# Optimization experiments

Measured on AMD Instinct MI355X. Metric: run time of the kernel, lower is better.

Reference implementation:

```python
import jax, jax.numpy as jnp
import numpy as np

B, N, HD = 4, 2048, 256
E, T = 4096, 1024
PROPAG_STEPS = 5
ALPHA_MAX = 0.2
LN_EPS = 1e-5


def setup_inputs() -> dict:
    key = jax.random.key(0)
    ks = jax.random.split(key, 16)
    s_in, s_h = (2.0 * HD) ** -0.5, HD ** -0.5
    return {
        "attr_matrix": jax.random.normal(ks[0], (B, N, 1), dtype=jnp.float32),
        "adj_matrix": jax.random.uniform(ks[1], (B, N, N), dtype=jnp.float32),
        # ggnn.linear_i: 1 -> HD
        "W_i": jax.random.normal(ks[2], (HD, 1), dtype=jnp.float32),
        "b_i": jnp.zeros((HD,), dtype=jnp.float32),
        # ggnn.gru: GRUCell(input=2*HD, hidden=HD), torch gate order r,z,n
        "W_ih": jax.random.normal(ks[3], (3 * HD, 2 * HD), dtype=jnp.float32) * s_in,
        "b_ih": jnp.zeros((3 * HD,), dtype=jnp.float32),
        "W_hh": jax.random.normal(ks[4], (3 * HD, HD), dtype=jnp.float32) * s_h,
        "b_hh": jnp.zeros((3 * HD,), dtype=jnp.float32),
        # ggnn.linear_o: HD -> 1
        "W_o": jax.random.normal(ks[5], (1, HD), dtype=jnp.float32) * s_h,
        "b_o": jnp.zeros((1,), dtype=jnp.float32),
        # topo buffers (incidence-like, kept small to mimic sparse +/-1 matrices)
        "B1": jax.random.normal(ks[6], (N, E), dtype=jnp.float32) * 0.02,
        "B2": jax.random.normal(ks[7], (E, T), dtype=jnp.float32) * 0.02,
        # topo trainables
        "proj_W": jax.random.normal(ks[8], (HD, HD), dtype=jnp.float32) * s_h,
        "ln_gamma": jnp.ones((HD,), dtype=jnp.float32),
        "ln_beta": jnp.zeros((HD,), dtype=jnp.float32),
        "alpha_raw": jnp.float32(-2.0),
    }


def _gru_cell(x, h, W_ih, b_ih, W_hh, b_hh):
    # x: [B,N,2H], h: [B,N,H]; torch GRUCell gate order: r, z, n
    gx = jnp.einsum('bni,gi->bng', x, W_ih) + b_ih
    gh = jnp.einsum('bnh,gh->bng', h, W_hh) + b_hh
    xr, xz, xn = jnp.split(gx, 3, axis=-1)
    hr, hz, hn = jnp.split(gh, 3, axis=-1)
    r = jax.nn.sigmoid(xr + hr)
    z = jax.nn.sigmoid(xz + hz)
    n = jnp.tanh(xn + r * hn)
    return (1.0 - z) * n + z * h


def _layernorm(x, gamma, beta):
    mu = jnp.mean(x, axis=-1, keepdims=True)
    var = jnp.mean(jnp.square(x - mu), axis=-1, keepdims=True)
    return (x - mu) * jax.lax.rsqrt(var + LN_EPS) * gamma + beta


def reference(attr_matrix, adj_matrix, W_i, b_i, W_ih, b_ih, W_hh, b_hh,
              W_o, b_o, B1, B2, proj_W, ln_gamma, ln_beta, alpha_raw):
    A_in = adj_matrix                      # [B,N,N]
    A_out = jnp.swapaxes(adj_matrix, -2, -1)
    # linear_i + relu
    h = jax.nn.relu(jnp.einsum('bnc,hc->bnh', attr_matrix, W_i) + b_i)  # [B,N,H]
    # GGNN propagation
    for _ in range(PROPAG_STEPS):
        a_in = jnp.einsum('bnm,bmh->bnh', A_in, h)
        a_out = jnp.einsum('bnm,bmh->bnh', A_out, h)
        h = _gru_cell(jnp.concatenate((a_in, a_out), axis=-1), h,
                      W_ih, b_ih, W_hh, b_hh)
    # topo residual: dH = B1 (L1 (B1^T h)), L1 = B1^T B1 + B2 B2^T
    L1 = B1.T @ B1 + B2 @ B2.T             # [E,E]
    E_feat = jnp.einsum('ne,bnh->beh', B1, h)       # B1^T H
    E_topo = jnp.einsum('ef,bfh->beh', L1, E_feat)
    dH = jnp.einsum('ne,beh->bnh', B1, E_topo)
    dH = _layernorm(jax.nn.relu(jnp.einsum('bnh,oh->bno', dH, proj_W)),
                    ln_gamma, ln_beta)
    alpha = ALPHA_MAX * jax.nn.sigmoid(alpha_raw)
    h = h + alpha * dH
    # linear_o -> [B,N] (squeeze(0) is a no-op for B>1)
    anomaly = (jnp.einsum('bnh,oh->bno', h, W_o) + b_o)[..., 0]
    return anomaly
```

## Files before the change

kernel.cpp:

```cpp
#include <hip/hip_runtime.h>


typedef __bf16 bf16x8 __attribute__((ext_vector_type(8)));
typedef float f32x4 __attribute__((ext_vector_type(4)));

#define BM 128
#define BN 128
#define BK 16

__device__ __forceinline__ unsigned short bf16rne(float x)
{
    unsigned u = __float_as_uint(x);
    return (unsigned short)((u + 0x7FFFu + ((u >> 16) & 1u)) >> 16);
}
__device__ __forceinline__ float bf2f(unsigned short h)
{
    return __uint_as_float((unsigned)h << 16);
}

__device__ __forceinline__ void split2(float x, unsigned short& hi, unsigned short& lo)
{
    hi = bf16rne(x);
    lo = bf16rne(x - bf2f(hi));
}

__device__ __forceinline__ void split3(float x, unsigned short& hi,
                                       unsigned short& md, unsigned short& lo)
{
    hi = bf16rne(x);
    float r = x - bf2f(hi);
    md = bf16rne(r);
    lo = bf16rne(r - bf2f(md));
}

__device__ __forceinline__ void gload_lds16(const unsigned short* g, unsigned short* l)
{
    __builtin_amdgcn_global_load_lds(
        (const __attribute__((address_space(1))) void*)g,
        (__attribute__((address_space(3))) void*)l, 16, 0, 0);
}

__device__ __forceinline__ void stage2(const unsigned short* g, unsigned short* l, int K)
{
    gload_lds16(g, l);
    gload_lds16(g + (size_t)32 * K, l + 2048);
}

template<int SPLIT>
__device__ __forceinline__ void mm_loop64(
    const unsigned short* ag0, const unsigned short* ag1, const unsigned short* ag2,
    const unsigned short* bg0, const unsigned short* bg1, const unsigned short* bg2,
    int K, unsigned short* LDS, int tid, f32x4 (&acc)[2][2])
{
    constexpr int NT = (SPLIT == 0) ? 1 : ((SPLIT == 4) ? 3 : 2);
    constexpr int TSZ = 4096;

    int lane = tid & 63, r16 = lane & 15, g = lane >> 4, s7 = r16 & 7;
    int wv = tid >> 6, wr = wv >> 1, wc = wv & 1;
    int arow = (wr * 32 + r16) * 128;
    int brow = (wc * 32 + r16) * 128;
    unsigned short* lA = LDS + (tid >> 6) * 512;
    unsigned short* lB = LDS + NT * TSZ + (tid >> 6) * 512;
    const char* Ab = (const char*)LDS;
    const char* Bb = (const char*)(LDS + NT * TSZ);

    for (int k0 = 0; k0 < K; k0 += 64) {
        stage2(ag0 + k0, lA, K);
        if constexpr (NT > 1) stage2(ag1 + k0, lA + TSZ, K);
        if constexpr (NT > 2) stage2(ag2 + k0, lA + 2 * TSZ, K);
        stage2(bg0 + k0, lB, K);
        if constexpr (NT > 1) stage2(bg1 + k0, lB + TSZ, K);
        if constexpr (NT > 2) stage2(bg2 + k0, lB + 2 * TSZ, K);
        __syncthreads();
#pragma unroll
        for (int ks = 0; ks < 2; ++ks) {
            int tt = ((ks * 4 + g) ^ s7) * 16;
            bf16x8 a0[2], a1[2], a2[2], b0[2], b1[2], b2[2];
#pragma unroll
            for (int mi = 0; mi < 2; ++mi) {
                a0[mi] = *(const bf16x8*)(Ab + arow + mi * 2048 + tt);
                if constexpr (NT > 1)
                    a1[mi] = *(const bf16x8*)(Ab + TSZ * 2 + arow + mi * 2048 + tt);
                if constexpr (NT > 2)
                    a2[mi] = *(const bf16x8*)(Ab + TSZ * 4 + arow + mi * 2048 + tt);
            }
#pragma unroll
            for (int ni = 0; ni < 2; ++ni) {
                b0[ni] = *(const bf16x8*)(Bb + brow + ni * 2048 + tt);
                if constexpr (NT > 1)
                    b1[ni] = *(const bf16x8*)(Bb + TSZ * 2 + brow + ni * 2048 + tt);
                if constexpr (NT > 2)
                    b2[ni] = *(const bf16x8*)(Bb + TSZ * 4 + brow + ni * 2048 + tt);
            }
#pragma unroll
            for (int mi = 0; mi < 2; ++mi)
#pragma unroll
                for (int ni = 0; ni < 2; ++ni) {
                    if constexpr (SPLIT == 4) {
                        acc[mi][ni] = __builtin_amdgcn_mfma_f32_16x16x32_bf16(
                            a2[mi], b0[ni], acc[mi][ni], 0, 0, 0);
                        acc[mi][ni] = __builtin_amdgcn_mfma_f32_16x16x32_bf16(
                            a0[mi], b2[ni], acc[mi][ni], 0, 0, 0);
                        acc[mi][ni] = __builtin_amdgcn_mfma_f32_16x16x32_bf16(
                            a1[mi], b1[ni], acc[mi][ni], 0, 0, 0);
                        acc[mi][ni] = __builtin_amdgcn_mfma_f32_16x16x32_bf16(
                            a1[mi], b0[ni], acc[mi][ni], 0, 0, 0);
                        acc[mi][ni] = __builtin_amdgcn_mfma_f32_16x16x32_bf16(
                            a0[mi], b1[ni], acc[mi][ni], 0, 0, 0);
                    } else if constexpr (SPLIT == 1 || SPLIT == 2) {
                        acc[mi][ni] = __builtin_amdgcn_mfma_f32_16x16x32_bf16(
                            a1[mi], b0[ni], acc[mi][ni], 0, 0, 0);
                        acc[mi][ni] = __builtin_amdgcn_mfma_f32_16x16x32_bf16(
                            a0[mi], b1[ni], acc[mi][ni], 0, 0, 0);
                        if constexpr (SPLIT == 2)
                            acc[mi][ni] = __builtin_amdgcn_mfma_f32_16x16x32_bf16(
                                a1[mi], b1[ni], acc[mi][ni], 0, 0, 0);
                    }
                    acc[mi][ni] = __builtin_amdgcn_mfma_f32_16x16x32_bf16(
                        a0[mi], b0[ni], acc[mi][ni], 0, 0, 0);
                }
        }
        __syncthreads();
    }
}

template<int SPLIT, int OBF>
__global__ __launch_bounds__(256, 2) void mm_bf16(
    const unsigned short* __restrict__ Ah, const unsigned short* __restrict__ A2,
    const unsigned short* __restrict__ A3,
    const unsigned short* __restrict__ Bh, const unsigned short* __restrict__ B2,
    const unsigned short* __restrict__ B3,
    int K, const float* __restrict__ bias, const float* __restrict__ Cacc,
    void* __restrict__ Cout, int ldc)
{
    constexpr int NT = (SPLIT == 0) ? 1 : ((SPLIT == 4) ? 3 : 2);
    __shared__ unsigned short LDS[2 * NT * 4096];
    int tid = threadIdx.x;

    unsigned nwg = gridDim.x * gridDim.y;
    unsigned lin = blockIdx.y * gridDim.x + blockIdx.x;
    unsigned wk = ((nwg & 7) == 0) ? (lin & 7) * (nwg >> 3) + (lin >> 3) : lin;
    unsigned bx = wk % gridDim.x, by = wk / gridDim.x;

    int m0 = by * 64, n0 = bx * 64;
    int rp = tid >> 3, sl8 = ((tid & 7) ^ (rp & 7)) * 8;
    const unsigned short* ag0 = Ah + (size_t)(m0 + rp) * K + sl8;
    const unsigned short* ag1 = (NT > 1) ? A2 + (size_t)(m0 + rp) * K + sl8 : nullptr;
    const unsigned short* ag2 = (NT > 2) ? A3 + (size_t)(m0 + rp) * K + sl8 : nullptr;
    const unsigned short* bg0 = Bh + (size_t)(n0 + rp) * K + sl8;
    const unsigned short* bg1 = (NT > 1) ? B2 + (size_t)(n0 + rp) * K + sl8 : nullptr;
    const unsigned short* bg2 = (NT > 2) ? B3 + (size_t)(n0 + rp) * K + sl8 : nullptr;

    f32x4 acc[2][2];
#pragma unroll
    for (int mi = 0; mi < 2; ++mi)
#pragma unroll
        for (int ni = 0; ni < 2; ++ni)
            acc[mi][ni] = (f32x4){0.f, 0.f, 0.f, 0.f};

    mm_loop64<SPLIT>(ag0, ag1, ag2, bg0, bg1, bg2, K, LDS, tid, acc);

    int lane = tid & 63, r16 = lane & 15, g = lane >> 4;
    int wv = tid >> 6, wr = wv >> 1, wc = wv & 1;
#pragma unroll
    for (int mi = 0; mi < 2; ++mi) {
#pragma unroll
        for (int ni = 0; ni < 2; ++ni) {
            int col = n0 + wc * 32 + ni * 16 + r16;
            float badd = bias ? bias[col] : 0.f;
#pragma unroll
            for (int j = 0; j < 4; ++j) {
                int row = m0 + wr * 32 + mi * 16 + g * 4 + j;
                float v = acc[mi][ni][j] + badd;
                if (Cacc) v += Cacc[(size_t)row * ldc + col];
                if (OBF)
                    ((unsigned short*)Cout)[(size_t)row * ldc + col] = bf16rne(v);
                else
                    ((float*)Cout)[(size_t)row * ldc + col] = v;
            }
        }
    }
}

__global__ __launch_bounds__(256, 2) void mm_step1(
    const unsigned short* __restrict__ AhHi, const unsigned short* __restrict__ AhLo,
    const unsigned short* __restrict__ AtHi, const unsigned short* __restrict__ AtLo,
    const unsigned short* __restrict__ hTh, const unsigned short* __restrict__ hTl,
    unsigned short* __restrict__ Xhi, unsigned short* __restrict__ Xmd,
    unsigned short* __restrict__ Xlo,
    const unsigned short* __restrict__ hrmh, const unsigned short* __restrict__ hrml,
    const unsigned short* __restrict__ WhhH, const unsigned short* __restrict__ WhhL,
    const float* __restrict__ b_hh, float* __restrict__ ghb)
{
    __shared__ unsigned short LDS[16384];
    int tid = threadIdx.x;
    unsigned bid = blockIdx.x;
    int lane = tid & 63, r16 = lane & 15, g = lane >> 4;
    int wv = tid >> 6, wr = wv >> 1, wc = wv & 1;
    int rp = tid >> 3, sl8 = ((tid & 7) ^ (rp & 7)) * 8;

    if (bid < 1024) {
        unsigned lin = bid;
        unsigned wk = (lin & 7) * 128 + (lin >> 3);
        unsigned bz = wk >> 7, rem = wk & 127, by = rem >> 2, bx = rem & 3;
        int b = bz >> 1, wio = bz & 1;
        const unsigned short* Ahp = (wio ? AtHi : AhHi) + (size_t)b * 4194304;
        const unsigned short* Alp = (wio ? AtLo : AhLo) + (size_t)b * 4194304;
        size_t boff = (size_t)(b * 256 + bx * 64) * 2048;
        int m0 = by * 64;
        const int K = 2048;
        const unsigned short* ag0 = Ahp + (size_t)(m0 + rp) * K + sl8;
        const unsigned short* ag1 = Alp + (size_t)(m0 + rp) * K + sl8;
        const unsigned short* bg0 = hTh + boff + (size_t)rp * K + sl8;
        const unsigned short* bg1 = hTl + boff + (size_t)rp * K + sl8;

        f32x4 acc[2][2];
#pragma unroll
        for (int mi = 0; mi < 2; ++mi)
#pragma unroll
            for (int ni = 0; ni < 2; ++ni)
                acc[mi][ni] = (f32x4){0.f, 0.f, 0.f, 0.f};

        mm_loop64<1>(ag0, ag1, nullptr, bg0, bg1, nullptr, K, LDS, tid, acc);

        float* T = reinterpret_cast<float*>(LDS);
#pragma unroll
        for (int mi = 0; mi < 2; ++mi)
#pragma unroll
            for (int ni = 0; ni < 2; ++ni)
#pragma unroll
                for (int j = 0; j < 4; ++j)
                    T[(wr * 32 + mi * 16 + g * 4 + j) * 68 +
                      wc * 32 + ni * 16 + r16] = acc[mi][ni][j];
        __syncthreads();

        int row = tid >> 2, fq = tid & 3;
        const float* src = T + row * 68 + fq * 16;
        unsigned hw[8], mw[8], lw[8];
#pragma unroll
        for (int e = 0; e < 8; ++e) {
            unsigned short h0, m0_, l0, h1, m1_, l1;
            split3(src[2 * e], h0, m0_, l0);
            split3(src[2 * e + 1], h1, m1_, l1);
            hw[e] = (unsigned)h0 | ((unsigned)h1 << 16);
            mw[e] = (unsigned)m0_ | ((unsigned)m1_ << 16);
            lw[e] = (unsigned)l0 | ((unsigned)l1 << 16);
        }
        size_t base = ((size_t)(m0 + row) * 4 + b) * 512 + wio * 256 + bx * 64 + fq * 16;
        ((uint4*)(Xhi + base))[0] = (uint4){hw[0], hw[1], hw[2], hw[3]};
        ((uint4*)(Xhi + base))[1] = (uint4){hw[4], hw[5], hw[6], hw[7]};
        ((uint4*)(Xmd + base))[0] = (uint4){mw[0], mw[1], mw[2], mw[3]};
        ((uint4*)(Xmd + base))[1] = (uint4){mw[4], mw[5], mw[6], mw[7]};
        ((uint4*)(Xlo + base))[0] = (uint4){lw[0], lw[1], lw[2], lw[3]};
        ((uint4*)(Xlo + base))[1] = (uint4){lw[4], lw[5], lw[6], lw[7]};
    } else {
        unsigned gidx = bid - 1024;
        unsigned by = gidx / 12, bx = gidx % 12;
        int m0 = by * 64, n0 = bx * 64;
        const int K = 256;
        const unsigned short* ag0 = hrmh + (size_t)(m0 + rp) * K + sl8;
        const unsigned short* ag1 = hrml + (size_t)(m0 + rp) * K + sl8;
        const unsigned short* bg0 = WhhH + (size_t)(n0 + rp) * K + sl8;
        const unsigned short* bg1 = WhhL + (size_t)(n0 + rp) * K + sl8;

        f32x4 acc[2][2];
#pragma unroll
        for (int mi = 0; mi < 2; ++mi)
#pragma unroll
            for (int ni = 0; ni < 2; ++ni)
                acc[mi][ni] = (f32x4){0.f, 0.f, 0.f, 0.f};

        mm_loop64<2>(ag0, ag1, nullptr, bg0, bg1, nullptr, K, LDS, tid, acc);

#pragma unroll
        for (int mi = 0; mi < 2; ++mi) {
#pragma unroll
            for (int ni = 0; ni < 2; ++ni) {
                int col = n0 + wc * 32 + ni * 16 + r16;
                float badd = b_hh[col];
#pragma unroll
                for (int j = 0; j < 4; ++j) {
                    int row = m0 + wr * 32 + mi * 16 + g * 4 + j;
                    ghb[(size_t)row * 768 + col] = acc[mi][ni][j] + badd;
                }
            }
        }
    }
}

__global__ __launch_bounds__(256, 2) void gemm_f32(
    const float* __restrict__ A, const float* __restrict__ B, float* __restrict__ C,
    int M, int N, int K, int lda, int ldb, int ldc,
    long sA, long sB, long sC,
    const float* __restrict__ bias, int ta, int tb, int accum)
{
    int bz = blockIdx.z;
    int taEff = ta;
    if (ta == 2) {
        int b = bz >> 1, w = bz & 1;
        A += (long)b * sA; B += (long)b * sB; C += (long)b * sC + w * 256;
        taEff = w;
    } else {
        A += (long)bz * sA; B += (long)bz * sB; C += (long)bz * sC;
    }
    int m0 = blockIdx.y * BM, n0 = blockIdx.x * BN;

    __shared__ float As[BK][BM + 4];
    __shared__ float Bs[BK][BN + 4];

// ... 94 lines not shown
        ushort4 h, l;
        split2(v.x, h.x, l.x); split2(v.y, h.y, l.y);
        split2(v.z, h.z, l.z); split2(v.w, h.w, l.w);
        size_t o = (size_t)z * 4194304 + (size_t)(i0 + r) * 2048 + j0 + tx * 4;
        *(ushort4*)(nhi + o) = h; *(ushort4*)(nlo + o) = l;
        t[r][tx * 4 + 0] = v.x; t[r][tx * 4 + 1] = v.y;
        t[r][tx * 4 + 2] = v.z; t[r][tx * 4 + 3] = v.w;
    }
    __syncthreads();
#pragma unroll
    for (int i = 0; i < 4; ++i) {
        int r = ty * 4 + i;
        ushort4 h, l;
        split2(t[tx * 4 + 0][r], h.x, l.x);
        split2(t[tx * 4 + 1][r], h.y, l.y);
        split2(t[tx * 4 + 2][r], h.z, l.z);
        split2(t[tx * 4 + 3][r], h.w, l.w);
        size_t o = (size_t)z * 4194304 + (size_t)(j0 + r) * 2048 + i0 + tx * 4;
        *(ushort4*)(thi + o) = h; *(ushort4*)(tlo + o) = l;
    }
}

__global__ void split_h(const float* __restrict__ h,
                        unsigned short* __restrict__ hi, unsigned short* __restrict__ lo,
                        unsigned short* __restrict__ hrmh, unsigned short* __restrict__ hrml)
{
    __shared__ float t[64][68];
    int f0 = blockIdx.x * 64, n0 = blockIdx.y * 64;
    int tx = threadIdx.x & 15, ty = threadIdx.x >> 4;
#pragma unroll
    for (int i = 0; i < 4; ++i) {
        int r = ty * 4 + i;
        float4 v = *(const float4*)(h + (size_t)(n0 + r) * 1024 + f0 + tx * 4);
        t[r][tx * 4 + 0] = v.x; t[r][tx * 4 + 1] = v.y;
        t[r][tx * 4 + 2] = v.z; t[r][tx * 4 + 3] = v.w;
        if (hrmh) {
            ushort4 hh, ll;
            split2(v.x, hh.x, ll.x); split2(v.y, hh.y, ll.y);
            split2(v.z, hh.z, ll.z); split2(v.w, hh.w, ll.w);
            size_t o = (size_t)(n0 + r) * 1024 + f0 + tx * 4;
            *(ushort4*)(hrmh + o) = hh;
            *(ushort4*)(hrml + o) = ll;
        }
    }
    __syncthreads();
#pragma unroll
    for (int i = 0; i < 4; ++i) {
        int r = ty * 4 + i;
        ushort4 hh, ll;
        split2(t[tx * 4 + 0][r], hh.x, ll.x);
        split2(t[tx * 4 + 1][r], hh.y, ll.y);
        split2(t[tx * 4 + 2][r], hh.z, ll.z);
        split2(t[tx * 4 + 3][r], hh.w, ll.w);
        size_t o = (size_t)(f0 + r) * 2048 + n0 + tx * 4;
        *(ushort4*)(hi + o) = hh; *(ushort4*)(lo + o) = ll;
    }
}

__global__ void split_t(const float* __restrict__ in, unsigned short* __restrict__ outN,
                        unsigned short* __restrict__ outT, int R, int C)
{
    __shared__ float t[64][68];
    int i0 = blockIdx.y * 64, j0 = blockIdx.x * 64;
    int tx = threadIdx.x & 15, ty = threadIdx.x >> 4;
#pragma unroll
    for (int i = 0; i < 4; ++i) {
        int r = ty * 4 + i;
        float4 v = *(const float4*)(in + (size_t)(i0 + r) * C + j0 + tx * 4);
        ushort4 hh;
        hh.x = bf16rne(v.x); hh.y = bf16rne(v.y);
        hh.z = bf16rne(v.z); hh.w = bf16rne(v.w);
        *(ushort4*)(outN + (size_t)(i0 + r) * C + j0 + tx * 4) = hh;
        t[r][tx * 4 + 0] = v.x; t[r][tx * 4 + 1] = v.y;
        t[r][tx * 4 + 2] = v.z; t[r][tx * 4 + 3] = v.w;
    }
    __syncthreads();
#pragma unroll
    for (int i = 0; i < 4; ++i) {
        int r = ty * 4 + i;
        ushort4 hh;
        hh.x = bf16rne(t[tx * 4 + 0][r]);
        hh.y = bf16rne(t[tx * 4 + 1][r]);
        hh.z = bf16rne(t[tx * 4 + 2][r]);
        hh.w = bf16rne(t[tx * 4 + 3][r]);
        *(ushort4*)(outT + (size_t)(j0 + r) * R + i0 + tx * 4) = hh;
    }
}

__global__ void split_w3(const float* __restrict__ Wih, const float* __restrict__ Whh,
                         const float* __restrict__ pj,
                         unsigned short* __restrict__ WihH, unsigned short* __restrict__ WihM,
                         unsigned short* __restrict__ WihL,
                         unsigned short* __restrict__ WhhH, unsigned short* __restrict__ WhhL,
                         unsigned short* __restrict__ pjH)
{
    int i = blockIdx.x * 256 + threadIdx.x;
    if (i < 393216) {
        unsigned short h, m, l;
        split3(Wih[i], h, m, l);
        WihH[i] = h; WihM[i] = m; WihL[i] = l;
    } else if (i < 589824) {
        int j = i - 393216;
        unsigned short h, l;
        split2(Whh[j], h, l);
        WhhH[j] = h; WhhL[j] = l;
    } else {
        int j = i - 589824;
        pjH[j] = bf16rne(pj[j]);
    }
}

__global__ __launch_bounds__(256, 3) void adj_mfma(
    const unsigned short* __restrict__ AhHi, const unsigned short* __restrict__ AhLo,
    const unsigned short* __restrict__ AtHi, const unsigned short* __restrict__ AtLo,
    const unsigned short* __restrict__ hTHi, const unsigned short* __restrict__ hTLo,
    float* __restrict__ c0, float* __restrict__ c1, float* __restrict__ c2)
{
    __shared__ unsigned short As[8192];
    __shared__ unsigned short Bs[8192];
    int tid = threadIdx.x;
    int bz = blockIdx.z;
    int region = bz >> 3, bw = bz & 7, b = bw >> 1, w = bw & 1;
    const unsigned short* Abase =
        (region == 2) ? (w ? AtLo : AhLo) : (w ? AtHi : AhHi);
    Abase += (size_t)b * 4194304;
    const unsigned short* Bbase = (region == 1) ? hTLo : hTHi;
    float* Cb = (region == 0) ? c0 : (region == 1 ? c1 : c2);

    int m0 = blockIdx.y * 128;
    int f0 = b * 256 + blockIdx.x * 128;

// ... 183 lines not shown
    const float* B1    = (const float*)d_in[10];
    const float* B2    = (const float*)d_in[11];
    const float* projW = (const float*)d_in[12];
    const float* gamma = (const float*)d_in[13];
    const float* beta  = (const float*)d_in[14];
    const float* araw  = (const float*)d_in[15];
    float* out = (float*)d_out;

    char* wsb = (char*)d_ws;
    dim3 blk(256);

    const size_t REQ1 = 0xD400000;
    const size_t REQ2 = 0xD000000;

    if (ws_size >= REQ1) {
        float* hbuf = (float*)(wsb);
        float* gxb  = (float*)(wsb + 0x0800000);
        unsigned short* hrmh = (unsigned short*)(wsb + 0x0800000);
        unsigned short* hrml = (unsigned short*)(wsb + 0x0C00000);
        unsigned short* hTh  = (unsigned short*)(wsb + 0x1800000);
        unsigned short* hTl  = (unsigned short*)(wsb + 0x1C00000);
        float* ghb  = (float*)(wsb + 0x2000000);
        unsigned short* Xhi = (unsigned short*)(wsb + 0x3800000);
        unsigned short* Xmd = (unsigned short*)(wsb + 0x4000000);
        unsigned short* Xlo = (unsigned short*)(wsb + 0x4800000);
        unsigned short* Wih_h = (unsigned short*)(wsb + 0x5000000);
        unsigned short* Wih_m = (unsigned short*)(wsb + 0x50C0000);
        unsigned short* Wih_l = (unsigned short*)(wsb + 0x5180000);
        unsigned short* Whh_h = (unsigned short*)(wsb + 0x5240000);
        unsigned short* Whh_l = (unsigned short*)(wsb + 0x52A0000);
        unsigned short* pjh   = (unsigned short*)(wsb + 0x5300000);
        char* R1 = wsb + 0x5400000;
        unsigned short* AhHi = (unsigned short*)(R1);
        unsigned short* AhLo = (unsigned short*)(R1 + 0x2000000);
        unsigned short* AtHi = (unsigned short*)(R1 + 0x4000000);
        unsigned short* AtLo = (unsigned short*)(R1 + 0x6000000);
        unsigned short* B1h = (unsigned short*)(R1);
        unsigned short* B1T = (unsigned short*)(R1 + 0x1000000);
        unsigned short* B2h = (unsigned short*)(R1 + 0x2000000);
        unsigned short* B2T = (unsigned short*)(R1 + 0x2800000);
        unsigned short* uTb = (unsigned short*)(R1 + 0x3000000);
        unsigned short* pTb = (unsigned short*)(R1 + 0x3800000);
        unsigned short* rTb = (unsigned short*)(R1 + 0x3C00000);
        unsigned short* qTb = (unsigned short*)(R1 + 0x3E00000);
        float* qTf = gxb;
        unsigned short* dHb = (unsigned short*)(wsb + 0x1800000);
        float* dPb = ghb;

        init_h<<<dim3(2048, 4), blk, 0, stream>>>(attr, W_i, b_i, hbuf);
        split_adj<<<dim3(32, 32, 4), blk, 0, stream>>>(adj, AhHi, AhLo, AtHi, AtLo);
        split_w3<<<dim3(2560), blk, 0, stream>>>(W_ih, W_hh, projW,
            Wih_h, Wih_m, Wih_l, Whh_h, Whh_l, pjh);

        for (int step = 0; step < 5; ++step) {
            split_h<<<dim3(16, 32), blk, 0, stream>>>(hbuf, hTh, hTl, hrmh, hrml);
            mm_step1<<<dim3(2560), blk, 0, stream>>>(
                AhHi, AhLo, AtHi, AtLo, hTh, hTl, Xhi, Xmd, Xlo,
                hrmh, hrml, Whh_h, Whh_l, b_hh, ghb);
            mm_bf16<4, 0><<<dim3(12, 128), blk, 0, stream>>>(
                Xhi, Xmd, Xlo, Wih_h, Wih_m, Wih_l,
                512, b_ih, nullptr, gxb, 768);
            gru_ew<<<dim3(2048, 4), blk, 0, stream>>>(gxb, ghb, hbuf);
        }

        split_h<<<dim3(16, 32), blk, 0, stream>>>(hbuf, hTh, hTl, nullptr, nullptr);
        split_t<<<dim3(64, 32), blk, 0, stream>>>(B1, B1h, B1T, 2048, 4096);
        split_t<<<dim3(16, 64), blk, 0, stream>>>(B2, B2h, B2T, 4096, 1024);
        mm_bf16<0, 1><<<dim3(64, 16), blk, 0, stream>>>(
            hTh, nullptr, nullptr, B1T, nullptr, nullptr,
            2048, nullptr, nullptr, uTb, 4096);
        mm_bf16<0, 1><<<dim3(32, 16), blk, 0, stream>>>(
            uTb, nullptr, nullptr, B1h, nullptr, nullptr,
            4096, nullptr, nullptr, pTb, 2048);
        mm_bf16<0, 1><<<dim3(16, 16), blk, 0, stream>>>(
            uTb, nullptr, nullptr, B2T, nullptr, nullptr,
            4096, nullptr, nullptr, rTb, 1024);
        mm_bf16<0, 0><<<dim3(64, 16), blk, 0, stream>>>(
            pTb, nullptr, nullptr, B1T, nullptr, nullptr,
            2048, nullptr, nullptr, qTf, 4096);
        mm_bf16<0, 1><<<dim3(64, 16), blk, 0, stream>>>(
            rTb, nullptr, nullptr, B2h, nullptr, nullptr,
            1024, nullptr, qTf, qTb, 4096);
        mm_bf16<0, 1><<<dim3(16, 32), blk, 0, stream>>>(
            B1h, nullptr, nullptr, qTb, nullptr, nullptr,
            4096, nullptr, nullptr, dHb, 1024);
        mm_bf16<0, 0><<<dim3(4, 128), blk, 0, stream>>>(
            dHb, nullptr, nullptr, pjh, nullptr, nullptr,
            256, nullptr, nullptr, dPb, 256);

        ln_out<<<dim3(2048, 4), blk, 0, stream>>>(dPb, gamma, beta, araw,
                                                  hbuf, W_o, b_o, out);
        return;
    }

    float* hbuf = (float*)(wsb);
    float* xbuf = (float*)(wsb + 0x800000);
    float* gxb  = (float*)(wsb + 0x1800000);
    float* ghb  = (float*)(wsb + 0x3000000);
    unsigned short* AhHi = (unsigned short*)(wsb + 0x4800000);
    unsigned short* AhLo = (unsigned short*)(wsb + 0x6800000);
    unsigned short* AtHi = (unsigned short*)(wsb + 0x8800000);
    unsigned short* AtLo = (unsigned short*)(wsb + 0xA800000);
    unsigned short* hTHi = (unsigned short*)(wsb + 0xC800000);
    unsigned short* hTLo = (unsigned short*)(wsb + 0xCC00000);

    float* ub  = xbuf;
    float* pb  = gxb;
    float* qb  = gxb + (1 << 21);
    float* rb  = ghb;
    float* dHr = ghb + (1 << 20);
    float* dPb = ghb + 3 * (1 << 20);

    bool mfma_path = (ws_size >= REQ2);

    init_h<<<dim3(2048, 4), blk, 0, stream>>>(attr, W_i, b_i, hbuf);

    if (mfma_path)
        split_adj<<<dim3(32, 32, 4), blk, 0, stream>>>(adj, AhHi, AhLo, AtHi, AtLo);

    for (int step = 0; step < 5; ++step) {
        if (mfma_path) {
            split_h<<<dim3(16, 32), blk, 0, stream>>>(hbuf, hTHi, hTLo, nullptr, nullptr);
            adj_mfma<<<dim3(2, 16, 24), blk, 0, stream>>>(
                AhHi, AhLo, AtHi, AtLo, hTHi, hTLo, xbuf, gxb, ghb);
            reduce3<<<dim3(4096), blk, 0, stream>>>(
                (float4*)xbuf, (const float4*)gxb, (const float4*)ghb);
        } else {
            gemm_f32<<<dim3(2, 16, 8), blk, 0, stream>>>(
                adj, hbuf, xbuf, 2048, 256, 2048, 2048, 1024, 2048,
                (long)2048 * 2048, 256, 512, nullptr, 2, 0, 0);
        }
        gemm_f32<<<dim3(6, 64, 1), blk, 0, stream>>>(
            xbuf, W_ih, gxb, 8192, 768, 512, 512, 512, 768,
            0, 0, 0, b_ih, 0, 1, 0);
        gemm_f32<<<dim3(6, 64, 1), blk, 0, stream>>>(
            hbuf, W_hh, ghb, 8192, 768, 256, 256, 256, 768,
            0, 0, 0, b_hh, 0, 1, 0);
        gru_ew<<<dim3(2048, 4), blk, 0, stream>>>(gxb, ghb, hbuf);
    }

    gemm_f32<<<dim3(8, 32, 1), blk, 0, stream>>>(
        B1, hbuf, ub, 4096, 1024, 2048, 4096, 1024, 1024, 0, 0, 0, nullptr, 1, 0, 0);
    gemm_f32<<<dim3(8, 16, 1), blk, 0, stream>>>(
        B1, ub, pb, 2048, 1024, 4096, 4096, 1024, 1024, 0, 0, 0, nullptr, 0, 0, 0);
    gemm_f32<<<dim3(8, 32, 1), blk, 0, stream>>>(
// ... 14 lines not shown
```

Before: 921.5 us.

## Switch split-precision MFMA GEMMs from bf16 to scaled fp16 hi/lo pairs

Replaces the bf16 two- and three-term operand splits with fp16 hi/lo pairs, where the lo part is scaled by 1024 and accumulated separately. This cuts the three-way W_ih/X split to two terms (three MFMAs instead of five) and drops the lo*lo term in the W_hh GEMM. It also removes the middle split buffers and their stores. fp16's extra mantissa bits are meant to keep accuracy, at the risk of fp16 range overflow or underflow on inputs with large or tiny magnitudes.

```diff
diff --git a/kernel.cpp b/kernel.cpp
--- a/kernel.cpp
+++ b/kernel.cpp
@@ -1,12 +1,15 @@
 #include <hip/hip_runtime.h>
+#include <hip/hip_fp16.h>
 
 
 typedef __bf16 bf16x8 __attribute__((ext_vector_type(8)));
+typedef _Float16 f16x8 __attribute__((ext_vector_type(8)));
 typedef float f32x4 __attribute__((ext_vector_type(4)));
 
 #define BM 128
 #define BN 128
 #define BK 16
+#define LO_INV (1.f / 1024.f)
 
 __device__ __forceinline__ unsigned short bf16rne(float x)
 {
@@ -17,20 +20,24 @@
 {
     return __uint_as_float((unsigned)h << 16);
 }
-
 __device__ __forceinline__ void split2(float x, unsigned short& hi, unsigned short& lo)
 {
     hi = bf16rne(x);
     lo = bf16rne(x - bf2f(hi));
 }
 
-__device__ __forceinline__ void split3(float x, unsigned short& hi,
-                                       unsigned short& md, unsigned short& lo)
-{
-    hi = bf16rne(x);
-    float r = x - bf2f(hi);
-    md = bf16rne(r);
-    lo = bf16rne(r - bf2f(md));
+__device__ __forceinline__ unsigned short f16r(float x)
+{
+    return __half_as_ushort(__float2half(x));
+}
+__device__ __forceinline__ float f16f(unsigned short u)
+{
+    return __half2float(__ushort_as_half(u));
+}
+__device__ __forceinline__ void splitf(float x, unsigned short& hi, unsigned short& lo)
+{
+    hi = f16r(x);
+    lo = f16r((x - f16f(hi)) * 1024.f);
 }
 
 __device__ __forceinline__ void gload_lds16(const unsigned short* g, unsigned short* l)
@@ -47,12 +54,13 @@
 }
 
 template<int SPLIT>
-__device__ __forceinline__ void mm_loop64(
-    const unsigned short* ag0, const unsigned short* ag1, const unsigned short* ag2,
-    const unsigned short* bg0, const unsigned short* bg1, const unsigned short* bg2,
-    int K, unsigned short* LDS, int tid, f32x4 (&acc)[2][2])
-{
-    constexpr int NT = (SPLIT == 0) ? 1 : ((SPLIT == 4) ? 3 : 2);
+__device__ __forceinline__ void mm_loop64f(
+    const unsigned short* ag0, const unsigned short* ag1,
+    const unsigned short* bg0, const unsigned short* bg1,
+    int K, unsigned short* LDS, int tid,
+    f32x4 (&acc0)[2][2], f32x4 (&acc1)[2][2])
+{
+    constexpr int NT = SPLIT ? 2 : 1;
     constexpr int TSZ = 4096;
 
     int lane = tid & 63, r16 = lane & 15, g = lane >> 4, s7 = r16 & 7;
@@ -66,74 +74,52 @@
 
     for (int k0 = 0; k0 < K; k0 += 64) {
         stage2(ag0 + k0, lA, K);
-        if constexpr (NT > 1) stage2(ag1 + k0, lA + TSZ, K);
-        if constexpr (NT > 2) stage2(ag2 + k0, lA + 2 * TSZ, K);
+        if constexpr (SPLIT) stage2(ag1 + k0, lA + TSZ, K);
         stage2(bg0 + k0, lB, K);
-        if constexpr (NT > 1) stage2(bg1 + k0, lB + TSZ, K);
-        if constexpr (NT > 2) stage2(bg2 + k0, lB + 2 * TSZ, K);
+        if constexpr (SPLIT) stage2(bg1 + k0, lB + TSZ, K);
         __syncthreads();
 #pragma unroll
         for (int ks = 0; ks < 2; ++ks) {
             int tt = ((ks * 4 + g) ^ s7) * 16;
-            bf16x8 a0[2], a1[2], a2[2], b0[2], b1[2], b2[2];
+            f16x8 a0[2], a1[2], b0[2], b1[2];
 #pragma unroll
             for (int mi = 0; mi < 2; ++mi) {
-                a0[mi] = *(const bf16x8*)(Ab + arow + mi * 2048 + tt);
-                if constexpr (NT > 1)
-                    a1[mi] = *(const bf16x8*)(Ab + TSZ * 2 + arow + mi * 2048 + tt);
-                if constexpr (NT > 2)
-                    a2[mi] = *(const bf16x8*)(Ab + TSZ * 4 + arow + mi * 2048 + tt);
+                a0[mi] = *(const f16x8*)(Ab + arow + mi * 2048 + tt);
+                if constexpr (SPLIT)
+                    a1[mi] = *(const f16x8*)(Ab + TSZ * 2 + arow + mi * 2048 + tt);
             }
 #pragma unroll
             for (int ni = 0; ni < 2; ++ni) {
-                b0[ni] = *(const bf16x8*)(Bb + brow + ni * 2048 + tt);
-                if constexpr (NT > 1)
-                    b1[ni] = *(const bf16x8*)(Bb + TSZ * 2 + brow + ni * 2048 + tt);
-                if constexpr (NT > 2)
-                    b2[ni] = *(const bf16x8*)(Bb + TSZ * 4 + brow + ni * 2048 + tt);
+                b0[ni] = *(const f16x8*)(Bb + brow + ni * 2048 + tt);
+                if constexpr (SPLIT)
+                    b1[ni] = *(const f16x8*)(Bb + TSZ * 2 + brow + ni * 2048 + tt);
             }
 #pragma unroll
             for (int mi = 0; mi < 2; ++mi)
 #pragma unroll
                 for (int ni = 0; ni < 2; ++ni) {
-                    if constexpr (SPLIT == 4) {
-                        acc[mi][ni] = __builtin_amdgcn_mfma_f32_16x16x32_bf16(
-                            a2[mi], b0[ni], acc[mi][ni], 0, 0, 0);
-                        acc[mi][ni] = __builtin_amdgcn_mfma_f32_16x16x32_bf16(
-                            a0[mi], b2[ni], acc[mi][ni], 0, 0, 0);
-                        acc[mi][ni] = __builtin_amdgcn_mfma_f32_16x16x32_bf16(
-                            a1[mi], b1[ni], acc[mi][ni], 0, 0, 0);
-                        acc[mi][ni] = __builtin_amdgcn_mfma_f32_16x16x32_bf16(
-                            a1[mi], b0[ni], acc[mi][ni], 0, 0, 0);
-                        acc[mi][ni] = __builtin_amdgcn_mfma_f32_16x16x32_bf16(
-                            a0[mi], b1[ni], acc[mi][ni], 0, 0, 0);
-                    } else if constexpr (SPLIT == 1 || SPLIT == 2) {
-                        acc[mi][ni] = __builtin_amdgcn_mfma_f32_16x16x32_bf16(
-                            a1[mi], b0[ni], acc[mi][ni], 0, 0, 0);
-                        acc[mi][ni] = __builtin_amdgcn_mfma_f32_16x16x32_bf16(
-                            a0[mi], b1[ni], acc[mi][ni], 0, 0, 0);
-                        if constexpr (SPLIT == 2)
-                            acc[mi][ni] = __builtin_amdgcn_mfma_f32_16x16x32_bf16(
-                                a1[mi], b1[ni], acc[mi][ni], 0, 0, 0);
+                    if constexpr (SPLIT) {
+                        acc1[mi][ni] = __builtin_amdgcn_mfma_f32_16x16x32_f16(
+                            a1[mi], b0[ni], acc1[mi][ni], 0, 0, 0);
+                        acc1[mi][ni] = __builtin_amdgcn_mfma_f32_16x16x32_f16(
+                            a0[mi], b1[ni], acc1[mi][ni], 0, 0, 0);
                     }
-                    acc[mi][ni] = __builtin_amdgcn_mfma_f32_16x16x32_bf16(
-                        a0[mi], b0[ni], acc[mi][ni], 0, 0, 0);
+                    acc0[mi][ni] = __builtin_amdgcn_mfma_f32_16x16x32_f16(
+                        a0[mi], b0[ni], acc0[mi][ni], 0, 0, 0);
                 }
         }
         __syncthreads();
     }
 }
 
-template<int SPLIT, int OBF>
-__global__ __launch_bounds__(256, 2) void mm_bf16(
-    const unsigned short* __restrict__ Ah, const unsigned short* __restrict__ A2,
-    const unsigned short* __restrict__ A3,
-    const unsigned short* __restrict__ Bh, const unsigned short* __restrict__ B2,
-    const unsigned short* __restrict__ B3,
+template<int SPLIT, int OF16>
+__global__ __launch_bounds__(256, 2) void mm_f16(
+    const unsigned short* __restrict__ Ah, const unsigned short* __restrict__ Al,
+    const unsigned short* __restrict__ Bh, const unsigned short* __restrict__ Bl,
     int K, const float* __restrict__ bias, const float* __restrict__ Cacc,
     void* __restrict__ Cout, int ldc)
 {
-    constexpr int NT = (SPLIT == 0) ? 1 : ((SPLIT == 4) ? 3 : 2);
+    constexpr int NT = SPLIT ? 2 : 1;
     __shared__ unsigned short LDS[2 * NT * 4096];
     int tid = threadIdx.x;
 
@@ -145,20 +131,20 @@
     int m0 = by * 64, n0 = bx * 64;
     int rp = tid >> 3, sl8 = ((tid & 7) ^ (rp & 7)) * 8;
     const unsigned short* ag0 = Ah + (size_t)(m0 + rp) * K + sl8;
-    const unsigned short* ag1 = (NT > 1) ? A2 + (size_t)(m0 + rp) * K + sl8 : nullptr;
-    const unsigned short* ag2 = (NT > 2) ? A3 + (size_t)(m0 + rp) * K + sl8 : nullptr;
+    const unsigned short* ag1 = SPLIT ? Al + (size_t)(m0 + rp) * K + sl8 : nullptr;
     const unsigned short* bg0 = Bh + (size_t)(n0 + rp) * K + sl8;
-    const unsigned short* bg1 = (NT > 1) ? B2 + (size_t)(n0 + rp) * K + sl8 : nullptr;
-    const unsigned short* bg2 = (NT > 2) ? B3 + (size_t)(n0 + rp) * K + sl8 : nullptr;
-
-    f32x4 acc[2][2];
+    const unsigned short* bg1 = SPLIT ? Bl + (size_t)(n0 + rp) * K + sl8 : nullptr;
+
+    f32x4 acc0[2][2], acc1[2][2];
 #pragma unroll
     for (int mi = 0; mi < 2; ++mi)
 #pragma unroll
-        for (int ni = 0; ni < 2; ++ni)
-            acc[mi][ni] = (f32x4){0.f, 0.f, 0.f, 0.f};
-
-    mm_loop64<SPLIT>(ag0, ag1, ag2, bg0, bg1, bg2, K, LDS, tid, acc);
+        for (int ni = 0; ni < 2; ++ni) {
+            acc0[mi][ni] = (f32x4){0.f, 0.f, 0.f, 0.f};
+            acc1[mi][ni] = (f32x4){0.f, 0.f, 0.f, 0.f};
+        }
+
+    mm_loop64f<SPLIT>(ag0, ag1, bg0, bg1, K, LDS, tid, acc0, acc1);
 
     int lane = tid & 63, r16 = lane & 15, g = lane >> 4;
     int wv = tid >> 6, wr = wv >> 1, wc = wv & 1;
@@ -171,10 +157,11 @@
 #pragma unroll
             for (int j = 0; j < 4; ++j) {
                 int row = m0 + wr * 32 + mi * 16 + g * 4 + j;
-                float v = acc[mi][ni][j] + badd;
+                float v = acc0[mi][ni][j] + badd;
+                if (SPLIT) v += acc1[mi][ni][j] * LO_INV;
                 if (Cacc) v += Cacc[(size_t)row * ldc + col];
-                if (OBF)
-                    ((unsigned short*)Cout)[(size_t)row * ldc + col] = bf16rne(v);
+                if (OF16)
+                    ((unsigned short*)Cout)[(size_t)row * ldc + col] = f16r(v);
                 else
                     ((float*)Cout)[(size_t)row * ldc + col] = v;
             }
@@ -182,12 +169,11 @@
     }
 }
 
-__global__ __launch_bounds__(256, 2) void mm_step1(
+__global__ __launch_bounds__(256, 2) void mm_step1f(
     const unsigned short* __restrict__ AhHi, const unsigned short* __restrict__ AhLo,
     const unsigned short* __restrict__ AtHi, const unsigned short* __restrict__ AtLo,
     const unsigned short* __restrict__ hTh, const unsigned short* __restrict__ hTl,
-    unsigned short* __restrict__ Xhi, unsigned short* __restrict__ Xmd,
-    unsigned short* __restrict__ Xlo,
+    unsigned short* __restrict__ Xhi, unsigned short* __restrict__ Xlo,
     const unsigned short* __restrict__ hrmh, const unsigned short* __restrict__ hrml,
     const unsigned short* __restrict__ WhhH, const unsigned short* __restrict__ WhhL,
     const float* __restrict__ b_hh, float* __restrict__ ghb)
@@ -199,9 +185,17 @@
     int wv = tid >> 6, wr = wv >> 1, wc = wv & 1;
     int rp = tid >> 3, sl8 = ((tid & 7) ^ (rp & 7)) * 8;
 
+    f32x4 acc0[2][2], acc1[2][2];
+#pragma unroll
+    for (int mi = 0; mi < 2; ++mi)
+#pragma unroll
+        for (int ni = 0; ni < 2; ++ni) {
+            acc0[mi][ni] = (f32x4){0.f, 0.f, 0.f, 0.f};
+            acc1[mi][ni] = (f32x4){0.f, 0.f, 0.f, 0.f};
+        }
+
     if (bid < 1024) {
-        unsigned lin = bid;
-        unsigned wk = (lin & 7) * 128 + (lin >> 3);
+        unsigned wk = (bid & 7) * 128 + (bid >> 3);
         unsigned bz = wk >> 7, rem = wk & 127, by = rem >> 2, bx = rem & 3;
         int b = bz >> 1, wio = bz & 1;
         const unsigned short* Ahp = (wio ? AtHi : AhHi) + (size_t)b * 4194304;
@@ -214,14 +208,7 @@
         const unsigned short* bg0 = hTh + boff + (size_t)rp * K + sl8;
         const unsigned short* bg1 = hTl + boff + (size_t)rp * K + sl8;
 
-        f32x4 acc[2][2];
-#pragma unroll
-        for (int mi = 0; mi < 2; ++mi)
-#pragma unroll
-            for (int ni = 0; ni < 2; ++ni)
-                acc[mi][ni] = (f32x4){0.f, 0.f, 0.f, 0.f};
-
-        mm_loop64<1>(ag0, ag1, nullptr, bg0, bg1, nullptr, K, LDS, tid, acc);
+        mm_loop64f<1>(ag0, ag1, bg0, bg1, K, LDS, tid, acc0, acc1);
 
         float* T = reinterpret_cast<float*>(LDS);
 #pragma unroll
@@ -231,26 +218,24 @@
 #pragma unroll
                 for (int j = 0; j < 4; ++j)
                     T[(wr * 32 + mi * 16 + g * 4 + j) * 68 +
-                      wc * 32 + ni * 16 + r16] = acc[mi][ni][j];
+                      wc * 32 + ni * 16 + r16] =
+                        acc0[mi][ni][j] + acc1[mi][ni][j] * LO_INV;
         __syncthreads();
 
         int row = tid >> 2, fq = tid & 3;
         const float* src = T + row * 68 + fq * 16;
-        unsigned hw[8], mw[8], lw[8];
+        unsigned hw[8], lw[8];
 #pragma unroll
         for (int e = 0; e < 8; ++e) {
-            unsigned short h0, m0_, l0, h1, m1_, l1;
-            split3(src[2 * e], h0, m0_, l0);
-            split3(src[2 * e + 1], h1, m1_, l1);
+            unsigned short h0, l0, h1, l1;
+            splitf(src[2 * e], h0, l0);
+            splitf(src[2 * e + 1], h1, l1);
             hw[e] = (unsigned)h0 | ((unsigned)h1 << 16);
-            mw[e] = (unsigned)m0_ | ((unsigned)m1_ << 16);
             lw[e] = (unsigned)l0 | ((unsigned)l1 << 16);
         }
         size_t base = ((size_t)(m0 + row) * 4 + b) * 512 + wio * 256 + bx * 64 + fq * 16;
         ((uint4*)(Xhi + base))[0] = (uint4){hw[0], hw[1], hw[2], hw[3]};
         ((uint4*)(Xhi + base))[1] = (uint4){hw[4], hw[5], hw[6], hw[7]};
-        ((uint4*)(Xmd + base))[0] = (uint4){mw[0], mw[1], mw[2], mw[3]};
-        ((uint4*)(Xmd + base))[1] = (uint4){mw[4], mw[5], mw[6], mw[7]};
         ((uint4*)(Xlo + base))[0] = (uint4){lw[0], lw[1], lw[2], lw[3]};
         ((uint4*)(Xlo + base))[1] = (uint4){lw[4], lw[5], lw[6], lw[7]};
     } else {
@@ -263,14 +248,7 @@
         const unsigned short* bg0 = WhhH + (size_t)(n0 + rp) * K + sl8;
         const unsigned short* bg1 = WhhL + (size_t)(n0 + rp) * K + sl8;
 
-        f32x4 acc[2][2];
-#pragma unroll
-        for (int mi = 0; mi < 2; ++mi)
-#pragma unroll
-            for (int ni = 0; ni < 2; ++ni)
-                acc[mi][ni] = (f32x4){0.f, 0.f, 0.f, 0.f};
-
-        mm_loop64<2>(ag0, ag1, nullptr, bg0, bg1, nullptr, K, LDS, tid, acc);
+        mm_loop64f<1>(ag0, ag1, bg0, bg1, K, LDS, tid, acc0, acc1);
 
 #pragma unroll
         for (int mi = 0; mi < 2; ++mi) {
@@ -281,10 +259,134 @@
 #pragma unroll
                 for (int j = 0; j < 4; ++j) {
                     int row = m0 + wr * 32 + mi * 16 + g * 4 + j;
-                    ghb[(size_t)row * 768 + col] = acc[mi][ni][j] + badd;
+                    ghb[(size_t)row * 768 + col] =
+                        acc0[mi][ni][j] + acc1[mi][ni][j] * LO_INV + badd;
                 }
             }
         }
+    }
+}
+
+__global__ void split_adj16(const float* __restrict__ adj,
+                            unsigned short* __restrict__ nhi, unsigned short* __restrict__ nlo,
+                            unsigned short* __restrict__ thi, unsigned short* __restrict__ tlo)
+{
+    __shared__ float t[64][68];
+    int z = blockIdx.z;
+    const float* src = adj + (size_t)z * 4194304;
+    int tx = threadIdx.x & 15, ty = threadIdx.x >> 4;
+    int i0 = blockIdx.y * 64, j0 = blockIdx.x * 64;
+#pragma unroll
+    for (int i = 0; i < 4; ++i) {
+        int r = ty * 4 + i;
+        float4 v = *(const float4*)(src + (size_t)(i0 + r) * 2048 + j0 + tx * 4);
+        ushort4 h, l;
+        splitf(v.x, h.x, l.x); splitf(v.y, h.y, l.y);
+        splitf(v.z, h.z, l.z); splitf(v.w, h.w, l.w);
+        size_t o = (size_t)z * 4194304 + (size_t)(i0 + r) * 2048 + j0 + tx * 4;
+        *(ushort4*)(nhi + o) = h; *(ushort4*)(nlo + o) = l;
+        t[r][tx * 4 + 0] = v.x; t[r][tx * 4 + 1] = v.y;
+        t[r][tx * 4 + 2] = v.z; t[r][tx * 4 + 3] = v.w;
+    }
+    __syncthreads();
+#pragma unroll
+    for (int i = 0; i < 4; ++i) {
+        int r = ty * 4 + i;
+        ushort4 h, l;
+        splitf(t[tx * 4 + 0][r], h.x, l.x);
+        splitf(t[tx * 4 + 1][r], h.y, l.y);
+        splitf(t[tx * 4 + 2][r], h.z, l.z);
+        splitf(t[tx * 4 + 3][r], h.w, l.w);
+        size_t o = (size_t)z * 4194304 + (size_t)(j0 + r) * 2048 + i0 + tx * 4;
+        *(ushort4*)(thi + o) = h; *(ushort4*)(tlo + o) = l;
+    }
+}
+
+__global__ void split_h16(const float* __restrict__ h,
+                          unsigned short* __restrict__ hi, unsigned short* __restrict__ lo,
+                          unsigned short* __restrict__ hrmh, unsigned short* __restrict__ hrml)
+{
+    __shared__ float t[64][68];
+    int f0 = blockIdx.x * 64, n0 = blockIdx.y * 64;
+    int tx = threadIdx.x & 15, ty = threadIdx.x >> 4;
+#pragma unroll
+    for (int i = 0; i < 4; ++i) {
+        int r = ty * 4 + i;
+        float4 v = *(const float4*)(h + (size_t)(n0 + r) * 1024 + f0 + tx * 4);
+        t[r][tx * 4 + 0] = v.x; t[r][tx * 4 + 1] = v.y;
+        t[r][tx * 4 + 2] = v.z; t[r][tx * 4 + 3] = v.w;
+        if (hrmh) {
+            ushort4 hh, ll;
+            splitf(v.x, hh.x, ll.x); splitf(v.y, hh.y, ll.y);
+            splitf(v.z, hh.z, ll.z); splitf(v.w, hh.w, ll.w);
+            size_t o = (size_t)(n0 + r) * 1024 + f0 + tx * 4;
+            *(ushort4*)(hrmh + o) = hh;
+            *(ushort4*)(hrml + o) = ll;
+        }
+    }
+    __syncthreads();
+#pragma unroll
+    for (int i = 0; i < 4; ++i) {
+        int r = ty * 4 + i;
+        ushort4 hh, ll;
+        splitf(t[tx * 4 + 0][r], hh.x, ll.x);
+        splitf(t[tx * 4 + 1][r], hh.y, ll.y);
+        splitf(t[tx * 4 + 2][r], hh.z, ll.z);
+        splitf(t[tx * 4 + 3][r], hh.w, ll.w);
+        size_t o = (size_t)(f0 + r) * 2048 + n0 + tx * 4;
+        *(ushort4*)(hi + o) = hh; *(ushort4*)(lo + o) = ll;
+    }
+}
+
+__global__ void split_t16(const float* __restrict__ in, unsigned short* __restrict__ outN,
+                          unsigned short* __restrict__ outT, int R, int C)
+{
+    __shared__ float t[64][68];
+    int i0 = blockIdx.y * 64, j0 = blockIdx.x * 64;
+    int tx = threadIdx.x & 15, ty = threadIdx.x >> 4;
+#pragma unroll
+    for (int i = 0; i < 4; ++i) {
+        int r = ty * 4 + i;
+        float4 v = *(const float4*)(in + (size_t)(i0 + r) * C + j0 + tx * 4);
+        ushort4 hh;
+        hh.x = f16r(v.x); hh.y = f16r(v.y);
+        hh.z = f16r(v.z); hh.w = f16r(v.w);
+        *(ushort4*)(outN + (size_t)(i0 + r) * C + j0 + tx * 4) = hh;
+        t[r][tx * 4 + 0] = v.x; t[r][tx * 4 + 1] = v.y;
+        t[r][tx * 4 + 2] = v.z; t[r][tx * 4 + 3] = v.w;
+    }
+    __syncthreads();
+#pragma unroll
+    for (int i = 0; i < 4; ++i) {
+        int r = ty * 4 + i;
+        ushort4 hh;
+        hh.x = f16r(t[tx * 4 + 0][r]);
+        hh.y = f16r(t[tx * 4 + 1][r]);
+        hh.z = f16r(t[tx * 4 + 2][r]);
+        hh.w = f16r(t[tx * 4 + 3][r]);
+        *(ushort4*)(outT + (size_t)(j0 + r) * R + i0 + tx * 4) = hh;
+    }
+}
+
+__global__ void split_w16(const float* __restrict__ Wih, const float* __restrict__ Whh,
+                          const float* __restrict__ pj,
+                          unsigned short* __restrict__ WihH, unsigned short* __restrict__ WihL,
+                          unsigned short* __restrict__ WhhH, unsigned short* __restrict__ WhhL,
+                          unsigned short* __restrict__ pjH)
+{
+    int i = blockIdx.x * 256 + threadIdx.x;
+    if (i < 393216) {
+        unsigned short h, l;
+        splitf(Wih[i], h, l);
+        WihH[i] = h; WihL[i] = l;
+    } else if (i < 589824) {
+        int j = i - 393216;
+        unsigned short h, l;
+        splitf(Whh[j], h, l);
+        WhhH[j] = h; WhhL[j] = l;
+    } else if (i < 655360) {
+        int j = i - 589824;
+        pjH[j] = f16r(pj[j]);
     }
 }
 
@@ -425,8 +527,7 @@
 }
 
 __global__ void split_h(const float* __restrict__ h,
-                        unsigned short* __restrict__ hi, unsigned short* __restrict__ lo,
-                        unsigned short* __restrict__ hrmh, unsigned short* __restrict__ hrml)
+                        unsigned short* __restrict__ hi, unsigned short* __restrict__ lo)
 {
     __shared__ float t[64][68];
     int f0 = blockIdx.x * 64, n0 = blockIdx.y * 64;
@@ -437,14 +538,6 @@
         float4 v = *(const float4*)(h + (size_t)(n0 + r) * 1024 + f0 + tx * 4);
         t[r][tx * 4 + 0] = v.x; t[r][tx * 4 + 1] = v.y;
         t[r][tx * 4 + 2] = v.z; t[r][tx * 4 + 3] = v.w;
-        if (hrmh) {
-            ushort4 hh, ll;
-            split2(v.x, hh.x, ll.x); split2(v.y, hh.y, ll.y);
-            split2(v.z, hh.z, ll.z); split2(v.w, hh.w, ll.w);
-            size_t o = (size_t)(n0 + r) * 1024 + f0 + tx * 4;
-            *(ushort4*)(hrmh + o) = hh;
-            *(ushort4*)(hrml + o) = ll;
-        }
     }
     __syncthreads();
 #pragma unroll
@@ -457,59 +550,6 @@
         split2(t[tx * 4 + 3][r], hh.w, ll.w);
         size_t o = (size_t)(f0 + r) * 2048 + n0 + tx * 4;
         *(ushort4*)(hi + o) = hh; *(ushort4*)(lo + o) = ll;
-    }
-}
-
-__global__ void split_t(const float* __restrict__ in, unsigned short* __restrict__ outN,
-                        unsigned short* __restrict__ outT, int R, int C)
-{
-    __shared__ float t[64][68];
-    int i0 = blockIdx.y * 64, j0 = blockIdx.x * 64;
-    int tx = threadIdx.x & 15, ty = threadIdx.x >> 4;
-#pragma unroll
-    for (int i = 0; i < 4; ++i) {
-        int r = ty * 4 + i;
-        float4 v = *(const float4*)(in + (size_t)(i0 + r) * C + j0 + tx * 4);
-        ushort4 hh;
-        hh.x = bf16rne(v.x); hh.y = bf16rne(v.y);
-        hh.z = bf16rne(v.z); hh.w = bf16rne(v.w);
-        *(ushort4*)(outN + (size_t)(i0 + r) * C + j0 + tx * 4) = hh;
-        t[r][tx * 4 + 0] = v.x; t[r][tx * 4 + 1] = v.y;
-        t[r][tx * 4 + 2] = v.z; t[r][tx * 4 + 3] = v.w;
-    }
-    __syncthreads();
-#pragma unroll
-    for (int i = 0; i < 4; ++i) {
-        int r = ty * 4 + i;
-        ushort4 hh;
-        hh.x = bf16rne(t[tx * 4 + 0][r]);
-        hh.y = bf16rne(t[tx * 4 + 1][r]);
-        hh.z = bf16rne(t[tx * 4 + 2][r]);
-        hh.w = bf16rne(t[tx * 4 + 3][r]);
-        *(ushort4*)(outT + (size_t)(j0 + r) * R + i0 + tx * 4) = hh;
-    }
-}
-
-__global__ void split_w3(const float* __restrict__ Wih, const float* __restrict__ Whh,
-                         const float* __restrict__ pj,
-                         unsigned short* __restrict__ WihH, unsigned short* __restrict__ WihM,
-                         unsigned short* __restrict__ WihL,
-                         unsigned short* __restrict__ WhhH, unsigned short* __restrict__ WhhL,
-                         unsigned short* __restrict__ pjH)
-{
-    int i = blockIdx.x * 256 + threadIdx.x;
-    if (i < 393216) {
-        unsigned short h, m, l;
-        split3(Wih[i], h, m, l);
-        WihH[i] = h; WihM[i] = m; WihL[i] = l;
-    } else if (i < 589824) {
-        int j = i - 393216;
-        unsigned short h, l;
-        split2(Whh[j], h, l);
-        WhhH[j] = h; WhhL[j] = l;
-    } else {
-        int j = i - 589824;
-        pjH[j] = bf16rne(pj[j]);
     }
 }
 
@@ -739,11 +779,9 @@
         unsigned short* hTl  = (unsigned short*)(wsb + 0x1C00000);
         float* ghb  = (float*)(wsb + 0x2000000);
         unsigned short* Xhi = (unsigned short*)(wsb + 0x3800000);
-        unsigned short* Xmd = (unsigned short*)(wsb + 0x4000000);
-        unsigned short* Xlo = (unsigned short*)(wsb + 0x4800000);
+        unsigned short* Xlo = (unsigned short*)(wsb + 0x4000000);
         unsigned short* Wih_h = (unsigned short*)(wsb + 0x5000000);
-        unsigned short* Wih_m = (unsigned short*)(wsb + 0x50C0000);
-        unsigned short* Wih_l = (unsigned short*)(wsb + 0x5180000);
+        unsigned short* Wih_l = (unsigned short*)(wsb + 0x50C0000);
         unsigned short* Whh_h = (unsigned short*)(wsb + 0x5240000);
         unsigned short* Whh_l = (unsigned short*)(wsb + 0x52A0000);
         unsigned short* pjh   = (unsigned short*)(wsb + 0x5300000);
@@ -765,45 +803,37 @@
         float* dPb = ghb;
 
         init_h<<<dim3(2048, 4), blk, 0, stream>>>(attr, W_i, b_i, hbuf);
-        split_adj<<<dim3(32, 32, 4), blk, 0, stream>>>(adj, AhHi, AhLo, AtHi, AtLo);
-        split_w3<<<dim3(2560), blk, 0, stream>>>(W_ih, W_hh, projW,
-            Wih_h, Wih_m, Wih_l, Whh_h, Whh_l, pjh);
+        split_adj16<<<dim3(32, 32, 4), blk, 0, stream>>>(adj, AhHi, AhLo, AtHi, AtLo);
+        split_w16<<<dim3(2560), blk, 0, stream>>>(W_ih, W_hh, projW,
+            Wih_h, Wih_l, Whh_h, Whh_l, pjh);
 
         for (int step = 0; step < 5; ++step) {
-            split_h<<<dim3(16, 32), blk, 0, stream>>>(hbuf, hTh, hTl, hrmh, hrml);
-            mm_step1<<<dim3(2560), blk, 0, stream>>>(
-                AhHi, AhLo, AtHi, AtLo, hTh, hTl, Xhi, Xmd, Xlo,
+            split_h16<<<dim3(16, 32), blk, 0, stream>>>(hbuf, hTh, hTl, hrmh, hrml);
+            mm_step1f<<<dim3(2560), blk, 0, stream>>>(
+                AhHi, AhLo, AtHi, AtLo, hTh, hTl, Xhi, Xlo,
                 hrmh, hrml, Whh_h, Whh_l, b_hh, ghb);
-            mm_bf16<4, 0><<<dim3(12, 128), blk, 0, stream>>>(
-                Xhi, Xmd, Xlo, Wih_h, Wih_m, Wih_l,
-                512, b_ih, nullptr, gxb, 768);
+            mm_f16<1, 0><<<dim3(12, 128), blk, 0, stream>>>(
+                Xhi, Xlo, Wih_h, Wih_l, 512, b_ih, nullptr, gxb, 768);
             gru_ew<<<dim3(2048, 4), blk, 0, stream>>>(gxb, ghb, hbuf);
         }
 
-        split_h<<<dim3(16, 32), blk, 0, stream>>>(hbuf, hTh, hTl, nullptr, nullptr);
-        split_t<<<dim3(64, 32), blk, 0, stream>>>(B1, B1h, B1T, 2048, 4096);
-        split_t<<<dim3(16, 64), blk, 0, stream>>>(B2, B2h, B2T, 4096, 1024);
-        mm_bf16<0, 1><<<dim3(64, 16), blk, 0, stream>>>(
-            hTh, nullptr, nullptr, B1T, nullptr, nullptr,
-            2048, nullptr, nullptr, uTb, 4096);
-        mm_bf16<0, 1><<<dim3(32, 16), blk, 0, stream>>>(
-            uTb, nullptr, nullptr, B1h, nullptr, nullptr,
-            4096, nullptr, nullptr, pTb, 2048);
-        mm_bf16<0, 1><<<dim3(16, 16), blk, 0, stream>>>(
-            uTb, nullptr, nullptr, B2T, nullptr, nullptr,
-            4096, nullptr, nullptr, rTb, 1024);
-        mm_bf16<0, 0><<<dim3(64, 16), blk, 0, stream>>>(
-            pTb, nullptr, nullptr, B1T, nullptr, nullptr,
-            2048, nullptr, nullptr, qTf, 4096);
-        mm_bf16<0, 1><<<dim3(64, 16), blk, 0, stream>>>(
-            rTb, nullptr, nullptr, B2h, nullptr, nullptr,
-            1024, nullptr, qTf, qTb, 4096);
-        mm_bf16<0, 1><<<dim3(16, 32), blk, 0, stream>>>(
-            B1h, nullptr, nullptr, qTb, nullptr, nullptr,
-            4096, nullptr, nullptr, dHb, 1024);
-        mm_bf16<0, 0><<<dim3(4, 128), blk, 0, stream>>>(
-            dHb, nullptr, nullptr, pjh, nullptr, nullptr,
-            256, nullptr, nullptr, dPb, 256);
+        split_h16<<<dim3(16, 32), blk, 0, stream>>>(hbuf, hTh, hTl, nullptr, nullptr);
+        split_t16<<<dim3(64, 32), blk, 0, stream>>>(B1, B1h, B1T, 2048, 4096);
+        split_t16<<<dim3(16, 64), blk, 0, stream>>>(B2, B2h, B2T, 4096, 1024);
+        mm_f16<0, 1><<<dim3(64, 16), blk, 0, stream>>>(
+            hTh, nullptr, B1T, nullptr, 2048, nullptr, nullptr, uTb, 4096);
+        mm_f16<0, 1><<<dim3(32, 16), blk, 0, stream>>>(
+            uTb, nullptr, B1h, nullptr, 4096, nullptr, nullptr, pTb, 2048);
+        mm_f16<0, 1><<<dim3(16, 16), blk, 0, stream>>>(
+            uTb, nullptr, B2T, nullptr, 4096, nullptr, nullptr, rTb, 1024);
+        mm_f16<0, 0><<<dim3(64, 16), blk, 0, stream>>>(
+            pTb, nullptr, B1T, nullptr, 2048, nullptr, nullptr, qTf, 4096);
+        mm_f16<0, 1><<<dim3(64, 16), blk, 0, stream>>>(
+            rTb, nullptr, B2h, nullptr, 1024, nullptr, qTf, qTb, 4096);
+        mm_f16<0, 1><<<dim3(16, 32), blk, 0, stream>>>(
+            B1h, nullptr, qTb, nullptr, 4096, nullptr, nullptr, dHb, 1024);
+        mm_f16<0, 0><<<dim3(4, 128), blk, 0, stream>>>(
+            dHb, nullptr, pjh, nullptr, 256, nullptr, nullptr, dPb, 256);
 
         ln_out<<<dim3(2048, 4), blk, 0, stream>>>(dPb, gamma, beta, araw,
                                                   hbuf, W_o, b_o, out);
@@ -837,7 +867,7 @@
 
     for (int step = 0; step < 5; ++step) {
         if (mfma_path) {
-            split_h<<<dim3(16, 32), blk, 0, stream>>>(hbuf, hTHi, hTLo, nullptr, nullptr);
+            split_h<<<dim3(16, 32), blk, 0, stream>>>(hbuf, hTHi, hTLo);
             adj_mfma<<<dim3(2, 16, 24), blk, 0, stream>>>(
                 AhHi, AhLo, AtHi, AtLo, hTHi, hTLo, xbuf, gxb, ghb);
             reduce3<<<dim3(4096), blk, 0, stream>>>(
```

Result: faster. 856.9 us (-7.0%).
